# Optimization experiments

Hardware: AMD Instinct MI355X
Metric: run time of the kernel (lower is better)

The kernel has to match this reference:

```python
import jax, jax.numpy as jnp
import numpy as np

B, N, H = 2, 1024, 768
MAX_W = 30
WIDTH_D = 20
SPAN_DIM = 3 * H + WIDTH_D  # 2324
K = int(N * 0.4)  # 409 (eval mode: // (1+0) )


def _enumerate_spans(n, max_w):
    # Replicates: enumerate_spans then sorted(spans[::-1], key=start)
    # -> start ascending, end DESCENDING within each start.
    spans = []
    for s in range(n):
        for e in range(min(s + max_w - 1, n - 1), s - 1, -1):
            spans.append((s, e))
    return np.asarray(spans, dtype=np.int32)  # [num_spans, 2]


def setup_inputs() -> dict:
    key = jax.random.key(0)
    ks = jax.random.split(key, 8)
    spans = jnp.asarray(_enumerate_spans(N, MAX_W))  # [30285, 2]
    return {
        "segment_embeddings": jax.random.normal(ks[0], (B, N, H), jnp.float32),
        "segment_mask": jnp.ones((B, N), jnp.int32),
        "candidate_spans": spans,
        "width_emb": jax.random.normal(ks[1], (MAX_W, WIDTH_D), jnp.float32) * 0.02,
        "W1": jax.random.normal(ks[2], (SPAN_DIM, H), jnp.float32) * 0.02,
        "b1": jax.random.normal(ks[3], (H,), jnp.float32) * 0.02,
        "w_s": jax.random.normal(ks[4], (H,), jnp.float32) * 0.02,
        "b_s": jax.random.normal(ks[5], (1,), jnp.float32) * 0.02,
        "k": K,
    }


def reference(segment_embeddings, segment_mask, candidate_spans, width_emb, W1, b1, w_s, b_s, k):
    starts = candidate_spans[:, 0]  # [S]
    ends = candidate_spans[:, 1]    # [S]
    # Endpoint span extractor: x, y, x*y + width embedding (width = end-start)
    x = segment_embeddings[:, starts, :]          # [B,S,H]
    y = segment_embeddings[:, ends, :]            # [B,S,H]
    wemb = width_emb[ends - starts]               # [S,WIDTH_D]
    bsz = segment_embeddings.shape[0]
    span_feat = jnp.concatenate(
        [x, y, x * y, jnp.broadcast_to(wemb[None], (bsz,) + wemb.shape)], axis=-1
    )  # [B,S,3H+WD]
    # MLP (dropout is identity in eval) + GELU (torch default: exact erf)
    h = jax.nn.gelu(jnp.einsum("bsd,dh->bsh", span_feat, W1) + b1, approximate=False)
    scores = jnp.einsum("bsh,h->bs", h, w_s) + b_s[0]  # [B,S]
    # Mask spans whose end index exceeds valid length
    lengths = segment_mask.sum(-1)  # [B]
    scores = scores + jnp.where(ends[None, :] >= lengths[:, None], -1e6, 0.0)
    # Top-k prune, then sort indices and gather
    _, idx = jax.lax.top_k(scores, k)          # [B,k]
    idx = jnp.sort(idx, axis=1)
    top_scores = jnp.take_along_axis(scores, idx, axis=1)            # [B,k]
    top_span_embs = jnp.take_along_axis(h, idx[:, :, None], axis=1)  # [B,k,H]
    top_spans = candidate_spans[idx]                                 # [B,k,2]
    return top_span_embs, top_scores, top_spans
```

## Files before the change

### kernel.cpp

```cpp
#include <hip/hip_runtime.h>
#include <math.h>

#define NB 2
#define NN 1024
#define HH 768
#define MAXW 30
#define KTOP 409
#define BANDCAP 4096
#define BAND_TAU 2e-2f
#define FILTCAP 6144
#define CHT 120
#define GPAD 448
#define SP416 416

typedef __attribute__((ext_vector_type(4))) float f32x4;
typedef __attribute__((ext_vector_type(8))) __bf16 bf16x8;
typedef __attribute__((ext_vector_type(8))) unsigned short us8;

constexpr int MT = 64, NT = 256, KT = 32;
constexpr int ASTR = MT + 4;
constexpr int BSTR = NT + 4;

__device__ __forceinline__ float gelu_f(float z) {
  return 0.5f * z * (1.0f + erff(z * 0.70710678118654752440f));
}
__device__ __forceinline__ unsigned f2key(float f) {
  unsigned u = __float_as_uint(f);
  return (u & 0x80000000u) ? ~u : (u | 0x80000000u);
}
__device__ __forceinline__ float key2f(unsigned k) {
  unsigned u = (k & 0x80000000u) ? (k & 0x7fffffffu) : ~k;
  return __uint_as_float(u);
}
__device__ __forceinline__ unsigned short f2bf_rn(float f) {
  unsigned u = __float_as_uint(f);
  unsigned r = u + 0x7fffu + ((u >> 16) & 1u);
  return (unsigned short)(r >> 16);
}
__device__ __forceinline__ float bf2f(unsigned short h) {
  return __uint_as_float(((unsigned)h) << 16);
}
__device__ __forceinline__ void async_copy16(const void* g, void* l) {
  __builtin_amdgcn_global_load_lds(
      (const __attribute__((address_space(1))) unsigned int*)g,
      (__attribute__((address_space(3))) unsigned int*)l, 16, 0, 0);
}

__global__ void len_kernel(const int* __restrict__ mask, int* __restrict__ lengths) {
  __shared__ int red[256];
  for (int b = 0; b < NB; ++b) {
    int s = 0;
    for (int i = threadIdx.x; i < NN; i += 256) s += mask[b * NN + i];
    red[threadIdx.x] = s;
    __syncthreads();
    for (int off = 128; off > 0; off >>= 1) {
      if (threadIdx.x < off) red[threadIdx.x] += red[threadIdx.x + off];
      __syncthreads();
    }
    if (threadIdx.x == 0) lengths[b] = red[0];
    __syncthreads();
  }
}

__global__ void r_kernel(const float* __restrict__ wemb, const float* __restrict__ W1,
                         const float* __restrict__ b1, float* __restrict__ R) {
  int w = blockIdx.x;
  for (int h = threadIdx.x; h < HH; h += 256) {
    float acc = b1[h];
    for (int j = 0; j < 20; ++j)
      acc = fmaf(wemb[w * 20 + j], W1[(size_t)(3 * HH + j) * HH + h], acc);
    R[w * HH + h] = acc;
  }
}

__global__ __launch_bounds__(256) void prep_bt_kernel(const float* __restrict__ W1,
                                                      unsigned short* __restrict__ Bt) {
  const int ki = blockIdx.x;
  const int hby = blockIdx.y;
  const float* W1c = W1 + (size_t)(2 * HH) * HH;
  const int t = threadIdx.x;
#pragma unroll
  for (int half = 0; half < 2; ++half) {
    const int c = t + half * 256;
    const int col = c >> 2, kg = c & 3;
    us8 v;
#pragma unroll
    for (int j = 0; j < 8; ++j) {
      const int k = ki * 32 + kg * 8 + j;
      v[j] = f2bf_rn(W1c[(size_t)k * HH + hby * 128 + col]);
    }
    *(us8*)(Bt + ((size_t)(hby * 24 + ki) * 512 + c) * 8) = v;
  }
}

__global__ __launch_bounds__(256) void prep_emb_hl_kernel(
    const float* __restrict__ emb, unsigned short* __restrict__ Ahi,
    unsigned short* __restrict__ Alo) {
  const int tile = blockIdx.x;
  const int ki = blockIdx.y;
  const int t = threadIdx.x;
#pragma unroll
  for (int half = 0; half < 2; ++half) {
    const int c = t + half * 256;
    const int row = c >> 2, kgs = c & 3;
    const int kg = kgs ^ ((row >> 1) & 3);
    const float* xr = emb + (size_t)(tile * 128 + row) * HH;
    const int k0 = ki * 32 + kg * 8;
    float4 x0 = *(const float4*)(xr + k0);
    float4 x1 = *(const float4*)(xr + k0 + 4);
    const float xv[8] = {x0.x, x0.y, x0.z, x0.w, x1.x, x1.y, x1.z, x1.w};
    us8 hv, lv;
#pragma unroll
    for (int j = 0; j < 8; ++j) {
      unsigned short h = f2bf_rn(xv[j]);
      hv[j] = h;
      lv[j] = f2bf_rn(xv[j] - bf2f(h));
    }
    const size_t base = (((size_t)tile * 24 + ki) * 512 + c) * 8;
    *(us8*)(Ahi + base) = hv;
    *(us8*)(Alo + base) = lv;
  }
}

__global__ __launch_bounds__(256) void prep_w1ab_kernel(
    const float* __restrict__ W1, unsigned short* __restrict__ Bhi,
    unsigned short* __restrict__ Blo) {
  const int ki = blockIdx.x;
  const int hby = blockIdx.y;
  const int t = threadIdx.x;
#pragma unroll
  for (int half = 0; half < 2; ++half) {
    const int c = t + half * 256;
    const int col = c >> 2, kg = c & 3;
    const int gc = hby * 128 + col;
    const float* base = W1 + (gc < 768 ? (size_t)0 : (size_t)HH * HH);
    const int n = (gc < 768) ? gc : gc - 768;
    us8 hv, lv;
#pragma unroll
    for (int j = 0; j < 8; ++j) {
      const int k = ki * 32 + kg * 8 + j;
      float v = base[(size_t)k * HH + n];
      unsigned short h = f2bf_rn(v);
      hv[j] = h;
      lv[j] = f2bf_rn(v - bf2f(h));
    }
    const size_t bo = (((size_t)hby * 24 + ki) * 512 + c) * 8;
    *(us8*)(Bhi + bo) = hv;
    *(us8*)(Blo + bo) = lv;
  }
}

__global__ __launch_bounds__(256) void pq_mfma_kernel(
    const unsigned short* __restrict__ Ahi, const unsigned short* __restrict__ Alo,
    const unsigned short* __restrict__ Bhi, const unsigned short* __restrict__ Blo,
    float* __restrict__ P, float* __restrict__ Q) {
  __shared__ unsigned short AsmH[128 * 32], AsmL[128 * 32];
  const int tile = blockIdx.x;
  const int hby = blockIdx.y;
  const int tid = threadIdx.x;
  const int lane = tid & 63, w = tid >> 6;
  const int wm = w & 1, wn = w >> 1;
  const int lm = lane & 15, lq = lane >> 4;

  f32x4 acc[4][4];
#pragma unroll
  for (int i = 0; i < 4; ++i)
#pragma unroll
    for (int j = 0; j < 4; ++j) acc[i][j] = (f32x4){0.f, 0.f, 0.f, 0.f};

  const unsigned short* AbH = Ahi + (size_t)tile * 24 * 4096;
  const unsigned short* AbL = Alo + (size_t)tile * 24 * 4096;
  const unsigned short* BbH = Bhi + (size_t)hby * 24 * 4096;
  const unsigned short* BbL = Blo + (size_t)hby * 24 * 4096;
  const int a_off = (wm * 64 + lm) * 32 + (lq ^ ((lm >> 1) & 3)) * 8;
  const int b_off = (wn * 64 + lm) * 32 + lq * 8;

  for (int ki = 0; ki < 24; ++ki) {
    async_copy16(AbH + (size_t)ki * 4096 + tid * 8, AsmH + tid * 8);
    async_copy16(AbH + (size_t)ki * 4096 + (tid + 256) * 8, AsmH + (tid + 256) * 8);
    async_copy16(AbL + (size_t)ki * 4096 + tid * 8, AsmL + tid * 8);
    async_copy16(AbL + (size_t)ki * 4096 + (tid + 256) * 8, AsmL + (tid + 256) * 8);
    bf16x8 bh[4], bl[4];
#pragma unroll
    for (int ni = 0; ni < 4; ++ni) {
      bh[ni] = *reinterpret_cast<const bf16x8*>(BbH + (size_t)ki * 4096 + b_off + ni * 512);
      bl[ni] = *reinterpret_cast<const bf16x8*>(BbL + (size_t)ki * 4096 + b_off + ni * 512);
    }
    __syncthreads();
    bf16x8 ah[4], al[4];
#pragma unroll
    for (int mi = 0; mi < 4; ++mi) {
      ah[mi] = *reinterpret_cast<const bf16x8*>(AsmH + a_off + mi * 512);
      al[mi] = *reinterpret_cast<const bf16x8*>(AsmL + a_off + mi * 512);
    }
#pragma unroll
    for (int ni = 0; ni < 4; ++ni)
#pragma unroll
      for (int mi = 0; mi < 4; ++mi) {
        acc[mi][ni] = __builtin_amdgcn_mfma_f32_16x16x32_bf16(ah[mi], bh[ni], acc[mi][ni], 0, 0, 0);
        acc[mi][ni] = __builtin_amdgcn_mfma_f32_16x16x32_bf16(ah[mi], bl[ni], acc[mi][ni], 0, 0, 0);
        acc[mi][ni] = __builtin_amdgcn_mfma_f32_16x16x32_bf16(al[mi], bh[ni], acc[mi][ni], 0, 0, 0);
      }
    __syncthreads();
  }

  float* Obase = (hby < 6) ? P : Q;
  const int cb = ((hby < 6) ? hby : hby - 6) * 128 + wn * 64 + lm;
  const int rowb = tile * 128 + wm * 64 + lq * 4;
#pragma unroll
  for (int mi = 0; mi < 4; ++mi)
#pragma unroll
    for (int ni = 0; ni < 4; ++ni)
#pragma unroll
      for (int r = 0; r < 4; ++r)
        Obase[(size_t)(rowb + mi * 16 + r) * HH + cb + ni * 16] = acc[mi][ni][r];
}

__global__ __launch_bounds__(256) void prep_a_kernel(
    const float* __restrict__ emb, const int* __restrict__ spans,
    unsigned short* __restrict__ At, int S, int tileofs) {
  const int tl = blockIdx.x, b = blockIdx.y;
  const int tile = tileofs + tl;
  const int t = threadIdx.x;
#pragma unroll
  for (int half = 0; half < 2; ++half) {
    const int c = t + half * 256;
    const int row = c >> 2, kgs = c & 3;
    const int kg = kgs ^ ((row >> 1) & 3);
    int g = tile * 128 + row;
    if (g >= S) g = S - 1;
    const int s = spans[2 * g], e = spans[2 * g + 1];
    const float* xr = emb + ((size_t)b * NN + s) * HH;
    const float* yr = emb + ((size_t)b * NN + e) * HH;
    unsigned short* dst = At + (((size_t)b * CHT + tl) * 24 * 512 + c) * 8;
    for (int ki = 0; ki < 24; ++ki) {
      const int k0 = ki * 32 + kg * 8;
      float4 x0 = *(const float4*)(xr + k0);
      float4 x1 = *(const float4*)(xr + k0 + 4);
      float4 y0 = *(const float4*)(yr + k0);
      float4 y1 = *(const float4*)(yr + k0 + 4);
      us8 v;
      v[0] = f2bf_rn(x0.x * y0.x); v[1] = f2bf_rn(x0.y * y0.y);
      v[2] = f2bf_rn(x0.z * y0.z); v[3] = f2bf_rn(x0.w * y0.w);
      v[4] = f2bf_rn(x1.x * y1.x); v[5] = f2bf_rn(x1.y * y1.y);
      v[6] = f2bf_rn(x1.z * y1.z); v[7] = f2bf_rn(x1.w * y1.w);
      *(us8*)(dst + (size_t)ki * 4096) = v;
    }
  }
}

__global__ __launch_bounds__(256, 3) void score_mfma3_kernel(
    const int* __restrict__ spans,
    const unsigned short* __restrict__ At, const unsigned short* __restrict__ Bt,
    const float* __restrict__ w_s,
    const float* __restrict__ P, const float* __restrict__ Q, const float* __restrict__ R,
    float* __restrict__ spart, int S, int tileofs) {
  __shared__ unsigned short Asm[128 * 32];
  __shared__ int ssm[128], eem[128], wwm[128];
  __shared__ float sred[128 * 2];

  const int tl = blockIdx.x;
  const int tile = tileofs + tl;
  const int hby = blockIdx.y;
  const int b = blockIdx.z;
  const int tid = threadIdx.x;
  const int lane = tid & 63, w = tid >> 6;
  const int wm = w & 1, wn = w >> 1;
  const int lm = lane & 15, lq = lane >> 4;

  if (tid < 128) {
    int g = tile * 128 + tid;
    int gg = g < S ? g : S - 1;
    int s = spans[2 * gg], e = spans[2 * gg + 1];
    ssm[tid] = s; eem[tid] = e; wwm[tid] = e - s;
  }

  f32x4 acc[4][4];
#pragma unroll
  for (int i = 0; i < 4; ++i)
#pragma unroll
    for (int j = 0; j < 4; ++j) acc[i][j] = (f32x4){0.f, 0.f, 0.f, 0.f};

  const unsigned short* Ab = At + ((size_t)b * CHT + tl) * 24 * 4096;
  const unsigned short* Bb = Bt + (size_t)hby * 24 * 4096;
  const int a_off = (wm * 64 + lm) * 32 + (lq ^ ((lm >> 1) & 3)) * 8;
  const int b_off = (wn * 64 + lm) * 32 + lq * 8;

  for (int ki = 0; ki < 24; ++ki) {
    async_copy16(Ab + (size_t)ki * 4096 + tid * 8, Asm + tid * 8);
    async_copy16(Ab + (size_t)ki * 4096 + (tid + 256) * 8, Asm + (tid + 256) * 8);
    bf16x8 bfr[4];
#pragma unroll
    for (int ni = 0; ni < 4; ++ni)
      bfr[ni] = *reinterpret_cast<const bf16x8*>(Bb + (size_t)ki * 4096 + b_off + ni * 512);
    __syncthreads();
    bf16x8 afr[4];
#pragma unroll
    for (int mi = 0; mi < 4; ++mi)
      afr[mi] = *reinterpret_cast<const bf16x8*>(Asm + a_off + mi * 512);
#pragma unroll
    for (int ni = 0; ni < 4; ++ni)
#pragma unroll
      for (int mi = 0; mi < 4; ++mi)
        acc[mi][ni] = __builtin_amdgcn_mfma_f32_16x16x32_bf16(afr[mi], bfr[ni], acc[mi][ni], 0, 0, 0);
    __syncthreads();
  }

  const int hbg = hby * 128;
  float wsv[4];
#pragma unroll
  for (int ni = 0; ni < 4; ++ni) wsv[ni] = w_s[hbg + wn * 64 + ni * 16 + lm];

#pragma unroll
  for (int mi = 0; mi < 4; ++mi) {
#pragma unroll
    for (int r = 0; r < 4; ++r) {
      const int rowl = wm * 64 + mi * 16 + lq * 4 + r;
      const int s = ssm[rowl], e = eem[rowl], wd = wwm[rowl];
      const float* Pp = P + ((size_t)b * NN + s) * HH + hbg + wn * 64 + lm;
      const float* Qp = Q + ((size_t)b * NN + e) * HH + hbg + wn * 64 + lm;
      const float* Rp = R + (size_t)wd * HH + hbg + wn * 64 + lm;
      float psum = 0.f;
#pragma unroll
      for (int ni = 0; ni < 4; ++ni) {
        float z = acc[mi][ni][r] + Pp[ni * 16] + Qp[ni * 16] + Rp[ni * 16];
        psum = fmaf(gelu_f(z), wsv[ni], psum);
      }
      psum += __shfl_xor(psum, 1);
      psum += __shfl_xor(psum, 2);
      psum += __shfl_xor(psum, 4);
      psum += __shfl_xor(psum, 8);
      if (lm == 0) sred[rowl * 2 + wn] = psum;
    }
  }
  __syncthreads();
  if (tid < 128) {
    int g = tile * 128 + tid;
    if (g < S)
      spart[(size_t)hby * ((size_t)NB * S) + (size_t)b * S + g] = sred[tid * 2] + sred[tid * 2 + 1];
  }
}

__global__ void combine_kernel(const float* __restrict__ sp, const int* __restrict__ spans,
                               const float* __restrict__ b_s, const int* __restrict__ lengths,
                               float* __restrict__ scores, int S) {
  int idx = blockIdx.x * 256 + threadIdx.x;
  if (idx >= NB * S) return;
  int b = idx / S, i = idx - b * S;
  size_t st = (size_t)NB * S;
  float v = b_s[0];
#pragma unroll
  for (int j = 0; j < 6; ++j) v += sp[j * st + idx];
  if (spans[2 * i + 1] >= lengths[b]) v += -1000000.0f;
  scores[idx] = v;
}

__global__ void zero_kernel(unsigned* __restrict__ hist, int* __restrict__ bandcount,
                            int* __restrict__ filtcount) {
  int i = blockIdx.x * 256 + threadIdx.x;
  hist[i] = 0;
  if (blockIdx.x == 0 && threadIdx.x < NB) {
    bandcount[threadIdx.x] = 0;
    filtcount[threadIdx.x] = 0;
  }
}

__global__ void hist16_kernel(const float* __restrict__ scores, unsigned* __restrict__ hist,
                              int S) {
  int idx = blockIdx.x * 256 + threadIdx.x;
  if (idx >= NB * S) return;
  int b = idx / S;
  unsigned key = f2key(scores[idx]) >> 16;
  atomicAdd(&hist[(size_t)b * 65536 + key], 1u);
}

__global__ __launch_bounds__(1024) void scan16_kernel(const unsigned* __restrict__ hist,
                                                      const int* __restrict__ kptr,
                                                      float* __restrict__ pivotf) {
  const int b = blockIdx.x;
  const unsigned* hb = hist + (size_t)b * 65536;
  const int tid = threadIdx.x;
  const unsigned k = (unsigned)kptr[0];
  __shared__ unsigned acc[1024];
  unsigned s = 0;
  for (int j = 0; j < 64; ++j) s += hb[tid * 64 + j];
  const unsigned mysum = s;
  acc[tid] = s;
  __syncthreads();
  for (int off = 1; off < 1024; off <<= 1) {
    unsigned v = (tid + off < 1024) ? acc[tid + off] : 0u;
    __syncthreads();
    acc[tid] += v;
    __syncthreads();
  }
  const unsigned above = acc[tid] - mysum;
  if (above < k && acc[tid] >= k) {
    unsigned cum = above;
    int binf = tid * 64;
    for (int j = 63; j >= 0; --j) {
      unsigned c = hb[tid * 64 + j];
      if (cum + c >= k) { binf = tid * 64 + j; break; }
      cum += c;
    }
    pivotf[b] = key2f(((unsigned)binf) << 16);
  }
}

__global__ void band_kernel(const float* __restrict__ scores, const float* __restrict__ pivotf,
                            int* __restrict__ bandcount, int* __restrict__ bandlist, int S) {
  int idx = blockIdx.x * 256 + threadIdx.x;
  if (idx >= NB * S) return;
  int b = idx / S, i = idx - b * S;
  if (fabsf(scores[idx] - pivotf[b]) <= BAND_TAU) {
    int slot = atomicAdd(&bandcount[b], 1);
    if (slot < BANDCAP) bandlist[b * BANDCAP + slot] = i;
  }
}

__global__ __launch_bounds__(256) void rescore_kernel(
    const float* __restrict__ emb, const int* __restrict__ spans,
    const float* __restrict__ W1, const float* __restrict__ w_s,
    const float* __restrict__ b_s, const int* __restrict__ lengths,
    const float* __restrict__ P, const float* __restrict__ Q, const float* __restrict__ R,
    const int* __restrict__ bandcount, const int* __restrict__ bandlist,
    float* __restrict__ scores, int S) {
  const int b = blockIdx.y;
  int cnt = bandcount[b];
  if (cnt > BANDCAP) cnt = BANDCAP;
  if ((int)blockIdx.x >= cnt) return;
  const int i = bandlist[b * BANDCAP + blockIdx.x];
  const int s = spans[2 * i], e = spans[2 * i + 1], wd = e - s;
  const int tid = threadIdx.x;
  __shared__ float prod[HH];
  __shared__ float red[256];
  for (int c = tid; c < HH; c += 256)
    prod[c] = emb[((size_t)b * NN + s) * HH + c] * emb[((size_t)b * NN + e) * HH + c];
  __syncthreads();
  const float* W1c = W1 + (size_t)(2 * HH) * HH;
  float psum = 0.f;
  for (int c0 = 0; c0 < HH; c0 += 256) {
    const int c = c0 + tid;
    float a = P[((size_t)b * NN + s) * HH + c] + Q[((size_t)b * NN + e) * HH + c] + R[(size_t)wd * HH + c];
    for (int k = 0; k < HH; ++k) a = fmaf(prod[k], W1c[(size_t)k * HH + c], a);
    psum = fmaf(gelu_f(a), w_s[c], psum);
  }
  red[tid] = psum;
  __syncthreads();
  for (int off = 128; off > 0; off >>= 1) {
    if (tid < off) red[tid] += red[tid + off];
    __syncthreads();
  }
  if (tid == 0) {
    float v = red[0] + b_s[0];
    if (e >= lengths[b]) v += -1000000.0f;
    scores[(size_t)b * S + i] = v;
  }
}

__global__ void filt_kernel(const float* __restrict__ scores, const float* __restrict__ pivotf,
                            int* __restrict__ filtcount, int* __restrict__ filtlist, int S) {
  int idx = blockIdx.x * 256 + threadIdx.x;
  if (idx >= NB * S) return;
  int b = idx / S, i = idx - b * S;
  if (scores[idx] > pivotf[b] - 0.01f) {
    int slot = atomicAdd(&filtcount[b], 1);
    if (slot < FILTCAP) filtlist[b * FILTCAP + slot] = i;
  }
}

__global__ __launch_bounds__(1024) void sel_kernel(
    const float* __restrict__ scores, const int* __restrict__ spans,
    const int* __restrict__ kptr, const int* __restrict__ filtcount,
    const int* __restrict__ filtlist,
    float* __restrict__ out_spans, int* __restrict__ sel, int S) {
  const int b = blockIdx.x;
  const int tid = threadIdx.x;
  const int k = kptr[0];
  __shared__ unsigned keys[FILTCAP];
  __shared__ int idxs[FILTCAP];
  __shared__ unsigned hist[256];
  __shared__ unsigned sh_prefix;
  __shared__ int sh_remaining;
  __shared__ int selcnt;
  __shared__ int slist[512];

  int M = filtcount[b];
  if (M > FILTCAP) M = FILTCAP;
  for (int i = tid; i < M; i += 1024) {
    int gi = filtlist[b * FILTCAP + i];
    idxs[i] = gi;
    keys[i] = f2key(scores[(size_t)b * S + gi]);
  }
  if (tid == 0) selcnt = 0;
  __syncthreads();

  unsigned prefix = 0;
  int remaining = k;
  for (int round = 0; round < 4; ++round) {
    const int shift = 24 - 8 * round;
    if (tid < 256) hist[tid] = 0;
    __syncthreads();
    for (int i = tid; i < M; i += 1024) {
      unsigned key = keys[i];
      if (round == 0 || (key >> (shift + 8)) == prefix)
        atomicAdd(&hist[(key >> shift) & 255u], 1u);
    }
    __syncthreads();
    if (tid == 0) {
      int cum = 0;
      for (int bin = 255; bin >= 0; --bin) {
        int c = (int)hist[bin];
        if (cum + c >= remaining) {
          sh_prefix = (prefix << 8) | (unsigned)bin;
          sh_remaining = remaining - cum;
          break;
        }
        cum += c;
      }
    }
    __syncthreads();
    prefix = sh_prefix;
    remaining = sh_remaining;
    __syncthreads();
  }
  const unsigned pk = prefix;
  const int m_eq = remaining;

  for (int i = tid; i < M; i += 1024) {
    unsigned key = keys[i];
    bool pick = false;
    if (key > pk) {
      pick = true;
    } else if (key == pk) {
      int r = 0;
      const int myidx = idxs[i];
      for (int j = 0; j < M; ++j)
        if (keys[j] == pk && idxs[j] < myidx) ++r;
      pick = (r < m_eq);
    }
    if (pick) {
      int p = atomicAdd(&selcnt, 1);
      if (p < 512) slist[p] = idxs[i];
    }
  }
  __syncthreads();

  for (int i = tid; i < k; i += 1024) {
    const int my = slist[i];
    int r = 0;
    for (int j = 0; j < k; ++j) r += (slist[j] < my);
    sel[b * KTOP + r] = my;
    out_spans[(b * KTOP + r) * 2 + 0] = (float)spans[2 * my];
    out_spans[(b * KTOP + r) * 2 + 1] = (float)spans[2 * my + 1];
  }
}

__global__ __launch_bounds__(256) void gather_part_kernel(
    const float* __restrict__ emb, const int* __restrict__ spans,
    const float* __restrict__ W1, const int* __restrict__ sel,
    float* __restrict__ Gpart) {
  __shared__ float As[KT][ASTR];
  __shared__ float Bs[KT][BSTR];
  __shared__ int ssm[MT], eem[MT];
  const int tile = blockIdx.x;
  const int hby6 = blockIdx.y;
  const int hb = (hby6 / 6) * NT;
  const int ks = hby6 % 6;
  const int b = blockIdx.z;
  const int tid = threadIdx.x;
  const int th = tid & 31, tw = tid >> 5;
  if (tid < MT) {
    int j = tile * MT + tid;
    if (j >= KTOP) j = KTOP - 1;
    int i = sel[b * KTOP + j];
    ssm[tid] = spans[2 * i];
    eem[tid] = spans[2 * i + 1];
  }
  __syncthreads();
  const int m0 = tid >> 3, m1 = m0 + 32;
  const int d0 = (tid & 7) << 2;
  const size_t ebase = (size_t)b * NN * HH;
  const size_t rx0 = ebase + (size_t)ssm[m0] * HH;
  const size_t ry0 = ebase + (size_t)eem[m0] * HH;
  const size_t rx1 = ebase + (size_t)ssm[m1] * HH;
  const size_t ry1 = ebase + (size_t)eem[m1] * HH;
  const float* W1c = W1 + (size_t)(2 * HH) * HH;
  const int bc = (tid & 63) << 2;
  const int br = tid >> 6;
  float acc[8][8];
#pragma unroll
  for (int i = 0; i < 8; ++i)
#pragma unroll
    for (int j = 0; j < 8; ++j) acc[i][j] = 0.f;
  const int k0 = ks * 128;
  for (int it = 0; it < 4; ++it) {
    const int kt = k0 + it * KT;
    float4 x0 = *reinterpret_cast<const float4*>(emb + rx0 + kt + d0);
    float4 y0 = *reinterpret_cast<const float4*>(emb + ry0 + kt + d0);
    float4 x1 = *reinterpret_cast<const float4*>(emb + rx1 + kt + d0);
    float4 y1 = *reinterpret_cast<const float4*>(emb + ry1 + kt + d0);
    float4 bw[8];
#pragma unroll
    for (int r = 0; r < 8; ++r)
      bw[r] = *reinterpret_cast<const float4*>(W1c + (size_t)(kt + br + 4 * r) * HH + hb + bc);
    __syncthreads();
    As[d0 + 0][m0] = x0.x * y0.x; As[d0 + 1][m0] = x0.y * y0.y;
    As[d0 + 2][m0] = x0.z * y0.z; As[d0 + 3][m0] = x0.w * y0.w;
    As[d0 + 0][m1] = x1.x * y1.x; As[d0 + 1][m1] = x1.y * y1.y;
    As[d0 + 2][m1] = x1.z * y1.z; As[d0 + 3][m1] = x1.w * y1.w;
#pragma unroll
    for (int r = 0; r < 8; ++r)
      *reinterpret_cast<float4*>(&Bs[br + 4 * r][bc]) = bw[r];
    __syncthreads();
#pragma unroll
    for (int d = 0; d < KT; ++d) {
      const float4 a0 = *reinterpret_cast<const float4*>(&As[d][tw * 4]);
      const float4 a1 = *reinterpret_cast<const float4*>(&As[d][tw * 4 + 32]);
      const float4 b0 = *reinterpret_cast<const float4*>(&Bs[d][th * 4]);
      const float4 b1v = *reinterpret_cast<const float4*>(&Bs[d][th * 4 + 128]);
      const float av[8] = {a0.x, a0.y, a0.z, a0.w, a1.x, a1.y, a1.z, a1.w};
      const float bv[8] = {b0.x, b0.y, b0.z, b0.w, b1v.x, b1v.y, b1v.z, b1v.w};
#pragma unroll
      for (int mi = 0; mi < 8; ++mi)
#pragma unroll
        for (int ni = 0; ni < 8; ++ni)
          acc[mi][ni] = fmaf(av[mi], bv[ni], acc[mi][ni]);
    }
  }
#pragma unroll
  for (int mi = 0; mi < 8; ++mi) {
    const int m = tw * 4 + (mi & 3) + ((mi >> 2) << 5);
    float* op = Gpart + (((size_t)ks * NB + b) * GPAD + tile * MT + m) * HH + hb;
    *reinterpret_cast<float4*>(op + th * 4) = make_float4(acc[mi][0], acc[mi][1], acc[mi][2], acc[mi][3]);
    *reinterpret_cast<float4*>(op + th * 4 + 128) = make_float4(acc[mi][4], acc[mi][5], acc[mi][6], acc[mi][7]);
  }
}

__global__ __launch_bounds__(256) void gather_fin_kernel(
    const float* __restrict__ Gpart, const int* __restrict__ spans,
    const int* __restrict__ sel,
    const float* __restrict__ P, const float* __restrict__ Q, const float* __restrict__ R,
    const float* __restrict__ w_s, float* __restrict__ outh, float* __restrict__ spartg) {
  __shared__ int ssm[16], eem[16], wwm[16], vvm[16];
  __shared__ float sred[16];
  const int t16 = blockIdx.x;
  const int hby = blockIdx.y;
  const int b = blockIdx.z;
  const int tid = threadIdx.x;
  if (tid < 16) {
    int j = t16 * 16 + tid;
    int valid = (j < KTOP) ? 1 : 0;
    int jj = valid ? j : KTOP - 1;
    int i = sel[b * KTOP + jj];
    ssm[tid] = spans[2 * i];
    eem[tid] = spans[2 * i + 1];
    wwm[tid] = eem[tid] - ssm[tid];
    vvm[tid] = valid;
  }
  __syncthreads();
  const int row = tid >> 4;
  const int cc = tid & 15;
  const int g448 = t16 * 16 + row;
  const int co = hby * 128 + cc * 8;
  float v[8];
#pragma unroll
  for (int i = 0; i < 8; ++i) v[i] = 0.f;
#pragma unroll
  for (int ks = 0; ks < 6; ++ks) {
    const float* gp = Gpart + (((size_t)ks * NB + b) * GPAD + g448) * HH + co;
    float4 a = *(const float4*)gp;
    float4 c = *(const float4*)(gp + 4);
    v[0] += a.x; v[1] += a.y; v[2] += a.z; v[3] += a.w;
    v[4] += c.x; v[5] += c.y; v[6] += c.z; v[7] += c.w;
  }
  const int s = ssm[row], e = eem[row], wd = wwm[row];
  const float* Pp = P + ((size_t)b * NN + s) * HH + co;
  const float* Qp = Q + ((size_t)b * NN + e) * HH + co;
  const float* Rp = R + (size_t)wd * HH + co;
  float4 p0 = *(const float4*)Pp, p1 = *(const float4*)(Pp + 4);
  float4 q0 = *(const float4*)Qp, q1 = *(const float4*)(Qp + 4);
  float4 r0 = *(const float4*)Rp, r1 = *(const float4*)(Rp + 4);
  v[0] += p0.x + q0.x + r0.x; v[1] += p0.y + q0.y + r0.y;
  v[2] += p0.z + q0.z + r0.z; v[3] += p0.w + q0.w + r0.w;
  v[4] += p1.x + q1.x + r1.x; v[5] += p1.y + q1.y + r1.y;
  v[6] += p1.z + q1.z + r1.z; v[7] += p1.w + q1.w + r1.w;
  float gl[8];
#pragma unroll
  for (int i = 0; i < 8; ++i) gl[i] = gelu_f(v[i]);
  float psum = 0.f;
  if (vvm[row]) {
    const int j = t16 * 16 + row;
    float* op = outh + (size_t)(b * KTOP + j) * HH + co;
    *(float4*)op = make_float4(gl[0], gl[1], gl[2], gl[3]);
    *(float4*)(op + 4) = make_float4(gl[4], gl[5], gl[6], gl[7]);
    const float4 w0 = *(const float4*)(w_s + co);
    const float4 w1 = *(const float4*)(w_s + co + 4);
    psum = gl[0] * w0.x + gl[1] * w0.y + gl[2] * w0.z + gl[3] * w0.w +
           gl[4] * w1.x + gl[5] * w1.y + gl[6] * w1.z + gl[7] * w1.w;
  }
  psum += __shfl_xor(psum, 1);
  psum += __shfl_xor(psum, 2);
  psum += __shfl_xor(psum, 4);
  psum += __shfl_xor(psum, 8);
  const int lane = tid & 63, wv = tid >> 6;
  if ((lane & 15) == 0) sred[wv * 4 + (lane >> 4)] = psum;
  __syncthreads();
  if (tid < 16)
    spartg[(size_t)hby * (NB * SP416) + b * SP416 + t16 * 16 + tid] = sred[tid];
}

__global__ void score_fin_kernel(const float* __restrict__ spartg, const int* __restrict__ sel,
                                 const int* __restrict__ spans, const float* __restrict__ b_s,
                                 const int* __restrict__ lengths, float* __restrict__ out_scores) {
  int idx = blockIdx.x * 256 + threadIdx.x;
  if (idx >= NB * KTOP) return;
  int b = idx / KTOP, j = idx - b * KTOP;
  float v = b_s[0];
#pragma unroll
  for (int hby = 0; hby < 6; ++hby)
    v += spartg[(size_t)hby * (NB * SP416) + b * SP416 + j];
  int i = sel[idx];
  if (spans[2 * i + 1] >= lengths[b]) v += -1000000.0f;
  out_scores[idx] = v;
}

extern "C" void kernel_launch(void* const* d_in, const int* in_sizes, int n_in,
                              void* d_out, int out_size, void* d_ws, size_t ws_size,
                              hipStream_t stream) {
  const float* emb = (const float*)d_in[0];
  const int* mask = (const int*)d_in[1];
  const int* spans = (const int*)d_in[2];
  const float* wemb = (const float*)d_in[3];
  const float* W1 = (const float*)d_in[4];
  const float* b1 = (const float*)d_in[5];
  const float* w_s = (const float*)d_in[6];
  const float* b_s = (const float*)d_in[7];
  const int* kptr = (const int*)d_in[8];
  const int S = in_sizes[2] / 2;
  float* out = (float*)d_out;

  char* wp = (char*)d_ws;
  auto take = [&](size_t bytes) {
    char* p = wp;
    wp += (bytes + 63) & ~(size_t)63;
    return p;
  };
  float* Pb = (float*)take((size_t)NB * NN * HH * 4);
  float* Qb = (float*)take((size_t)NB * NN * HH * 4);
  float* Rb = (float*)take((size_t)MAXW * HH * 4);
  float* spart = (float*)take(6 * (size_t)NB * S * 4);
  float* scoresb = (float*)take((size_t)NB * S * 4);
  float* spartg = (float*)take(6 * (size_t)NB * SP416 * 4);
  float* Gpart = (float*)take(6 * (size_t)NB * GPAD * HH * 4);
  float* pivotf = (float*)take(NB * 4);
  unsigned short* At = (unsigned short*)take((size_t)NB * CHT * 24 * 4096 * 2);
  unsigned short* Bt = (unsigned short*)take((size_t)6 * 24 * 4096 * 2);
  unsigned* hist16b = (unsigned*)take((size_t)NB * 65536 * 4);
  int* selb = (int*)take(NB * KTOP * 4);
  int* lengthsb = (int*)take(NB * 4);
  int* bandcount = (int*)take(NB * 4);
  int* bandlist = (int*)take((size_t)NB * BANDCAP * 4);
  int* filtcount = (int*)take(NB * 4);
  int* filtlist = (int*)take((size_t)NB * FILTCAP * 4);

  unsigned short* AimgHi = At;
  unsigned short* AimgLo = AimgHi + (size_t)16 * 24 * 4096;
  unsigned short* BimgHi = AimgLo + (size_t)16 * 24 * 4096;
  unsigned short* BimgLo = BimgHi + (size_t)12 * 24 * 4096;

  const size_t OFF1 = (size_t)NB * KTOP * HH;
  const size_t OFF2 = OFF1 + (size_t)NB * KTOP;

  const int tiles = (S + 127) / 128;

  len_kernel<<<dim3(1), dim3(256), 0, stream>>>(mask, lengthsb);
  r_kernel<<<dim3(MAXW), dim3(256), 0, stream>>>(wemb, W1, b1, Rb);
  prep_bt_kernel<<<dim3(24, 6), dim3(256), 0, stream>>>(W1, Bt);
  prep_emb_hl_kernel<<<dim3(16, 24), dim3(256), 0, stream>>>(emb, AimgHi, AimgLo);
  prep_w1ab_kernel<<<dim3(24, 12), dim3(256), 0, stream>>>(W1, BimgHi, BimgLo);
  pq_mfma_kernel<<<dim3(16, 12), dim3(256), 0, stream>>>(AimgHi, AimgLo, BimgHi, BimgLo, Pb, Qb);
  zero_kernel<<<dim3(512), dim3(256), 0, stream>>>(hist16b, bandcount, filtcount);

  for (int pass = 0; pass < 2; ++pass) {
    const int ofs = pass * CHT;
    const int nt = (pass == 0) ? CHT : (tiles - CHT);
    prep_a_kernel<<<dim3(nt, NB), dim3(256), 0, stream>>>(emb, spans, At, S, ofs);
    score_mfma3_kernel<<<dim3(nt, 6, NB), dim3(256), 0, stream>>>(
        spans, At, Bt, w_s, Pb, Qb, Rb, spart, S, ofs);
  }

  combine_kernel<<<dim3((NB * S + 255) / 256), dim3(256), 0, stream>>>(
      spart, spans, b_s, lengthsb, scoresb, S);
  hist16_kernel<<<dim3((NB * S + 255) / 256), dim3(256), 0, stream>>>(scoresb, hist16b, S);
  scan16_kernel<<<dim3(NB), dim3(1024), 0, stream>>>(hist16b, kptr, pivotf);
  band_kernel<<<dim3((NB * S + 255) / 256), dim3(256), 0, stream>>>(
      scoresb, pivotf, bandcount, bandlist, S);
  rescore_kernel<<<dim3(BANDCAP, NB), dim3(256), 0, stream>>>(
      emb, spans, W1, w_s, b_s, lengthsb, Pb, Qb, Rb, bandcount, bandlist, scoresb, S);
  filt_kernel<<<dim3((NB * S + 255) / 256), dim3(256), 0, stream>>>(
      scoresb, pivotf, filtcount, filtlist, S);
  sel_kernel<<<dim3(NB), dim3(1024), 0, stream>>>(
      scoresb, spans, kptr, filtcount, filtlist, out + OFF2, selb, S);
  gather_part_kernel<<<dim3(7, 18, NB), dim3(256), 0, stream>>>(emb, spans, W1, selb, Gpart);
  gather_fin_kernel<<<dim3(26, 6, NB), dim3(256), 0, stream>>>(
      Gpart, spans, selb, Pb, Qb, Rb, w_s, out, spartg);
  score_fin_kernel<<<dim3((NB * KTOP + 255) / 256), dim3(256), 0, stream>>>(
      spartg, selb, spans, b_s, lengthsb, out + OFF1);
}
```

Baseline: 560.3 us.

## Widen score MFMA tile to 256 columns and move gather GEMM to split-bf16 MFMA

The main scoring kernel now makes each block compute 256 output columns instead of 128. This halves the number of times each A tile is streamed and halves the partial-score reductions, at the cost of doubling the accumulator registers and lowering launch bounds occupancy from 3 to 2. The gather stage used an fp32 FMA GEMM followed by a separate partial-sum kernel. It is replaced by a bf16 hi/lo split MFMA GEMM (three products) that fuses GELU, the output write and the partial score computation. This needs a new prep kernel for the gathered A images and a low-part copy of the B image.

New measurement: 677.2 us. +20.9%, slower.

```diff
diff --git a/kernel.cpp b/kernel.cpp
--- a/kernel.cpp
+++ b/kernel.cpp
@@ -10,16 +10,11 @@
 #define BAND_TAU 2e-2f
 #define FILTCAP 6144
 #define CHT 120
-#define GPAD 448
-#define SP416 416
+#define GROWS 512
 
 typedef __attribute__((ext_vector_type(4))) float f32x4;
 typedef __attribute__((ext_vector_type(8))) __bf16 bf16x8;
 typedef __attribute__((ext_vector_type(8))) unsigned short us8;
-
-constexpr int MT = 64, NT = 256, KT = 32;
-constexpr int ASTR = MT + 4;
-constexpr int BSTR = NT + 4;
 
 __device__ __forceinline__ float gelu_f(float z) {
   return 0.5f * z * (1.0f + erff(z * 0.70710678118654752440f));
@@ -74,7 +69,8 @@
 }
 
 __global__ __launch_bounds__(256) void prep_bt_kernel(const float* __restrict__ W1,
-                                                      unsigned short* __restrict__ Bt) {
+                                                      unsigned short* __restrict__ Bt,
+                                                      unsigned short* __restrict__ Btlo) {
   const int ki = blockIdx.x;
   const int hby = blockIdx.y;
   const float* W1c = W1 + (size_t)(2 * HH) * HH;
@@ -83,13 +79,18 @@
   for (int half = 0; half < 2; ++half) {
     const int c = t + half * 256;
     const int col = c >> 2, kg = c & 3;
-    us8 v;
+    us8 hv, lv;
 #pragma unroll
     for (int j = 0; j < 8; ++j) {
       const int k = ki * 32 + kg * 8 + j;
-      v[j] = f2bf_rn(W1c[(size_t)k * HH + hby * 128 + col]);
-    }
-    *(us8*)(Bt + ((size_t)(hby * 24 + ki) * 512 + c) * 8) = v;
+      float v = W1c[(size_t)k * HH + hby * 128 + col];
+      unsigned short h = f2bf_rn(v);
+      hv[j] = h;
+      lv[j] = f2bf_rn(v - bf2f(h));
+    }
+    const size_t bo = ((size_t)(hby * 24 + ki) * 512 + c) * 8;
+    *(us8*)(Bt + bo) = hv;
+    *(us8*)(Btlo + bo) = lv;
   }
 }
 
@@ -249,7 +250,7 @@
   }
 }
 
-__global__ __launch_bounds__(256, 3) void score_mfma3_kernel(
+__global__ __launch_bounds__(256, 2) void score_mfma4_kernel(
     const int* __restrict__ spans,
     const unsigned short* __restrict__ At, const unsigned short* __restrict__ Bt,
     const float* __restrict__ w_s,
@@ -259,9 +260,9 @@
   __shared__ int ssm[128], eem[128], wwm[128];
   __shared__ float sred[128 * 2];
 
-  const int tl = blockIdx.x;
+  const int hb2 = blockIdx.x;
+  const int tl = blockIdx.y;
   const int tile = tileofs + tl;
-  const int hby = blockIdx.y;
   const int b = blockIdx.z;
   const int tid = threadIdx.x;
   const int lane = tid & 63, w = tid >> 6;
@@ -275,41 +276,45 @@
     ssm[tid] = s; eem[tid] = e; wwm[tid] = e - s;
   }
 
-  f32x4 acc[4][4];
+  f32x4 acc[4][8];
 #pragma unroll
   for (int i = 0; i < 4; ++i)
 #pragma unroll
-    for (int j = 0; j < 4; ++j) acc[i][j] = (f32x4){0.f, 0.f, 0.f, 0.f};
+    for (int j = 0; j < 8; ++j) acc[i][j] = (f32x4){0.f, 0.f, 0.f, 0.f};
 
   const unsigned short* Ab = At + ((size_t)b * CHT + tl) * 24 * 4096;
-  const unsigned short* Bb = Bt + (size_t)hby * 24 * 4096;
+  const unsigned short* Bb0 = Bt + (size_t)(hb2 * 2) * 24 * 4096;
+  const unsigned short* Bb1 = Bt + (size_t)(hb2 * 2 + 1) * 24 * 4096;
   const int a_off = (wm * 64 + lm) * 32 + (lq ^ ((lm >> 1) & 3)) * 8;
   const int b_off = (wn * 64 + lm) * 32 + lq * 8;
 
   for (int ki = 0; ki < 24; ++ki) {
     async_copy16(Ab + (size_t)ki * 4096 + tid * 8, Asm + tid * 8);
     async_copy16(Ab + (size_t)ki * 4096 + (tid + 256) * 8, Asm + (tid + 256) * 8);
-    bf16x8 bfr[4];
-#pragma unroll
-    for (int ni = 0; ni < 4; ++ni)
-      bfr[ni] = *reinterpret_cast<const bf16x8*>(Bb + (size_t)ki * 4096 + b_off + ni * 512);
+    bf16x8 bfr[8];
+#pragma unroll
+    for (int ni = 0; ni < 4; ++ni) {
+      bfr[ni] = *reinterpret_cast<const bf16x8*>(Bb0 + (size_t)ki * 4096 + b_off + ni * 512);
+      bfr[ni + 4] = *reinterpret_cast<const bf16x8*>(Bb1 + (size_t)ki * 4096 + b_off + ni * 512);
+    }
     __syncthreads();
     bf16x8 afr[4];
 #pragma unroll
     for (int mi = 0; mi < 4; ++mi)
       afr[mi] = *reinterpret_cast<const bf16x8*>(Asm + a_off + mi * 512);
 #pragma unroll
-    for (int ni = 0; ni < 4; ++ni)
+    for (int ni = 0; ni < 8; ++ni)
 #pragma unroll
       for (int mi = 0; mi < 4; ++mi)
         acc[mi][ni] = __builtin_amdgcn_mfma_f32_16x16x32_bf16(afr[mi], bfr[ni], acc[mi][ni], 0, 0, 0);
     __syncthreads();
   }
 
-  const int hbg = hby * 128;
-  float wsv[4];
-#pragma unroll
-  for (int ni = 0; ni < 4; ++ni) wsv[ni] = w_s[hbg + wn * 64 + ni * 16 + lm];
+  const int hbg = hb2 * 256;
+  float wsv[8];
+#pragma unroll
+  for (int ni = 0; ni < 8; ++ni)
+    wsv[ni] = w_s[hbg + (ni >> 2) * 128 + wn * 64 + (ni & 3) * 16 + lm];
 
 #pragma unroll
   for (int mi = 0; mi < 4; ++mi) {
@@ -322,8 +327,9 @@
       const float* Rp = R + (size_t)wd * HH + hbg + wn * 64 + lm;
       float psum = 0.f;
 #pragma unroll
-      for (int ni = 0; ni < 4; ++ni) {
-        float z = acc[mi][ni][r] + Pp[ni * 16] + Qp[ni * 16] + Rp[ni * 16];
+      for (int ni = 0; ni < 8; ++ni) {
+        const int co = (ni >> 2) * 128 + (ni & 3) * 16;
+        float z = acc[mi][ni][r] + Pp[co] + Qp[co] + Rp[co];
         psum = fmaf(gelu_f(z), wsv[ni], psum);
       }
       psum += __shfl_xor(psum, 1);
@@ -337,7 +343,7 @@
   if (tid < 128) {
     int g = tile * 128 + tid;
     if (g < S)
-      spart[(size_t)hby * ((size_t)NB * S) + (size_t)b * S + g] = sred[tid * 2] + sred[tid * 2 + 1];
+      spart[(size_t)hb2 * ((size_t)NB * S) + (size_t)b * S + g] = sred[tid * 2] + sred[tid * 2 + 1];
   }
 }
 
@@ -350,7 +356,7 @@
   size_t st = (size_t)NB * S;
   float v = b_s[0];
 #pragma unroll
-  for (int j = 0; j < 6; ++j) v += sp[j * st + idx];
+  for (int j = 0; j < 3; ++j) v += sp[j * st + idx];
   if (spans[2 * i + 1] >= lengths[b]) v += -1000000.0f;
   scores[idx] = v;
 }
@@ -555,100 +561,67 @@
   }
 }
 
-__global__ __launch_bounds__(256) void gather_part_kernel(
+__global__ __launch_bounds__(256) void prep_ga_kernel(
     const float* __restrict__ emb, const int* __restrict__ spans,
-    const float* __restrict__ W1, const int* __restrict__ sel,
-    float* __restrict__ Gpart) {
-  __shared__ float As[KT][ASTR];
-  __shared__ float Bs[KT][BSTR];
-  __shared__ int ssm[MT], eem[MT];
+    const int* __restrict__ sel, unsigned short* __restrict__ GAhi,
+    unsigned short* __restrict__ GAlo) {
   const int tile = blockIdx.x;
-  const int hby6 = blockIdx.y;
-  const int hb = (hby6 / 6) * NT;
-  const int ks = hby6 % 6;
-  const int b = blockIdx.z;
-  const int tid = threadIdx.x;
-  const int th = tid & 31, tw = tid >> 5;
-  if (tid < MT) {
-    int j = tile * MT + tid;
+  const int b = blockIdx.y;
+  const int t = threadIdx.x;
+#pragma unroll
+  for (int half = 0; half < 2; ++half) {
+    const int c = t + half * 256;
+    const int row = c >> 2, kgs = c & 3;
+    const int kg = kgs ^ ((row >> 1) & 3);
+    int j = tile * 128 + row;
     if (j >= KTOP) j = KTOP - 1;
-    int i = sel[b * KTOP + j];
-    ssm[tid] = spans[2 * i];
-    eem[tid] = spans[2 * i + 1];
-  }
-  __syncthreads();
-  const int m0 = tid >> 3, m1 = m0 + 32;
-  const int d0 = (tid & 7) << 2;
-  const size_t ebase = (size_t)b * NN * HH;
-  const size_t rx0 = ebase + (size_t)ssm[m0] * HH;
-  const size_t ry0 = ebase + (size_t)eem[m0] * HH;
-  const size_t rx1 = ebase + (size_t)ssm[m1] * HH;
-  const size_t ry1 = ebase + (size_t)eem[m1] * HH;
-  const float* W1c = W1 + (size_t)(2 * HH) * HH;
-  const int bc = (tid & 63) << 2;
-  const int br = tid >> 6;
-  float acc[8][8];
-#pragma unroll
-  for (int i = 0; i < 8; ++i)
-#pragma unroll
-    for (int j = 0; j < 8; ++j) acc[i][j] = 0.f;
-  const int k0 = ks * 128;
-  for (int it = 0; it < 4; ++it) {
-    const int kt = k0 + it * KT;
-    float4 x0 = *reinterpret_cast<const float4*>(emb + rx0 + kt + d0);
-    float4 y0 = *reinterpret_cast<const float4*>(emb + ry0 + kt + d0);
-    float4 x1 = *reinterpret_cast<const float4*>(emb + rx1 + kt + d0);
-    float4 y1 = *reinterpret_cast<const float4*>(emb + ry1 + kt + d0);
-    float4 bw[8];
-#pragma unroll
-    for (int r = 0; r < 8; ++r)
-      bw[r] = *reinterpret_cast<const float4*>(W1c + (size_t)(kt + br + 4 * r) * HH + hb + bc);
-    __syncthreads();
-    As[d0 + 0][m0] = x0.x * y0.x; As[d0 + 1][m0] = x0.y * y0.y;
-    As[d0 + 2][m0] = x0.z * y0.z; As[d0 + 3][m0] = x0.w * y0.w;
-    As[d0 + 0][m1] = x1.x * y1.x; As[d0 + 1][m1] = x1.y * y1.y;
-    As[d0 + 2][m1] = x1.z * y1.z; As[d0 + 3][m1] = x1.w * y1.w;
-#pragma unroll
-    for (int r = 0; r < 8; ++r)
-      *reinterpret_cast<float4*>(&Bs[br + 4 * r][bc]) = bw[r];
-    __syncthreads();
-#pragma unroll
-    for (int d = 0; d < KT; ++d) {
-      const float4 a0 = *reinterpret_cast<const float4*>(&As[d][tw * 4]);
-      const float4 a1 = *reinterpret_cast<const float4*>(&As[d][tw * 4 + 32]);
-      const float4 b0 = *reinterpret_cast<const float4*>(&Bs[d][th * 4]);
-      const float4 b1v = *reinterpret_cast<const float4*>(&Bs[d][th * 4 + 128]);
-      const float av[8] = {a0.x, a0.y, a0.z, a0.w, a1.x, a1.y, a1.z, a1.w};
-      const float bv[8] = {b0.x, b0.y, b0.z, b0.w, b1v.x, b1v.y, b1v.z, b1v.w};
-#pragma unroll
-      for (int mi = 0; mi < 8; ++mi)
-#pragma unroll
-        for (int ni = 0; ni < 8; ++ni)
-          acc[mi][ni] = fmaf(av[mi], bv[ni], acc[mi][ni]);
-    }
-  }
-#pragma unroll
-  for (int mi = 0; mi < 8; ++mi) {
-    const int m = tw * 4 + (mi & 3) + ((mi >> 2) << 5);
-    float* op = Gpart + (((size_t)ks * NB + b) * GPAD + tile * MT + m) * HH + hb;
-    *reinterpret_cast<float4*>(op + th * 4) = make_float4(acc[mi][0], acc[mi][1], acc[mi][2], acc[mi][3]);
-    *reinterpret_cast<float4*>(op + th * 4 + 128) = make_float4(acc[mi][4], acc[mi][5], acc[mi][6], acc[mi][7]);
-  }
-}
-
-__global__ __launch_bounds__(256) void gather_fin_kernel(
-    const float* __restrict__ Gpart, const int* __restrict__ spans,
-    const int* __restrict__ sel,
+    const int i = sel[b * KTOP + j];
+    const int s = spans[2 * i], e = spans[2 * i + 1];
+    const float* xr = emb + ((size_t)b * NN + s) * HH;
+    const float* yr = emb + ((size_t)b * NN + e) * HH;
+    unsigned short* dh = GAhi + (((size_t)(b * 4 + tile)) * 24 * 512 + c) * 8;
+    unsigned short* dl = GAlo + (((size_t)(b * 4 + tile)) * 24 * 512 + c) * 8;
+    for (int ki = 0; ki < 24; ++ki) {
+      const int k0 = ki * 32 + kg * 8;
+      float4 x0 = *(const float4*)(xr + k0);
+      float4 x1 = *(const float4*)(xr + k0 + 4);
+      float4 y0 = *(const float4*)(yr + k0);
+      float4 y1 = *(const float4*)(yr + k0 + 4);
+      const float pv[8] = {x0.x * y0.x, x0.y * y0.y, x0.z * y0.z, x0.w * y0.w,
+                           x1.x * y1.x, x1.y * y1.y, x1.z * y1.z, x1.w * y1.w};
+      us8 hv, lv;
+#pragma unroll
+      for (int q = 0; q < 8; ++q) {
+        unsigned short h = f2bf_rn(pv[q]);
+        hv[q] = h;
+        lv[q] = f2bf_rn(pv[q] - bf2f(h));
+      }
+      *(us8*)(dh + (size_t)ki * 4096) = hv;
+      *(us8*)(dl + (size_t)ki * 4096) = lv;
+    }
+  }
+}
+
+__global__ __launch_bounds__(256) void gather_mfma_kernel(
+    const int* __restrict__ spans, const int* __restrict__ sel,
+    const unsigned short* __restrict__ GAhi, const unsigned short* __restrict__ GAlo,
+    const unsigned short* __restrict__ Bt, const unsigned short* __restrict__ Btlo,
+    const float* __restrict__ w_s,
     const float* __restrict__ P, const float* __restrict__ Q, const float* __restrict__ R,
-    const float* __restrict__ w_s, float* __restrict__ outh, float* __restrict__ spartg) {
-  __shared__ int ssm[16], eem[16], wwm[16], vvm[16];
-  __shared__ float sred[16];
-  const int t16 = blockIdx.x;
+    float* __restrict__ outh, float* __restrict__ spartg) {
+  __shared__ unsigned short AsmH[128 * 32], AsmL[128 * 32];
+  __shared__ int ssm[128], eem[128], wwm[128], vvm[128];
+  __shared__ float sred[128 * 2];
+  const int tile = blockIdx.x;
   const int hby = blockIdx.y;
   const int b = blockIdx.z;
   const int tid = threadIdx.x;
-  if (tid < 16) {
-    int j = t16 * 16 + tid;
+  const int lane = tid & 63, w = tid >> 6;
+  const int wm = w & 1, wn = w >> 1;
+  const int lm = lane & 15, lq = lane >> 4;
+
+  if (tid < 128) {
+    int j = tile * 128 + tid;
     int valid = (j < KTOP) ? 1 : 0;
     int jj = valid ? j : KTOP - 1;
     int i = sel[b * KTOP + jj];
@@ -657,56 +630,84 @@
     wwm[tid] = eem[tid] - ssm[tid];
     vvm[tid] = valid;
   }
+
+  f32x4 acc[4][4];
+#pragma unroll
+  for (int i = 0; i < 4; ++i)
+#pragma unroll
+    for (int j = 0; j < 4; ++j) acc[i][j] = (f32x4){0.f, 0.f, 0.f, 0.f};
+
+  const unsigned short* AbH = GAhi + (size_t)(b * 4 + tile) * 24 * 4096;
+  const unsigned short* AbL = GAlo + (size_t)(b * 4 + tile) * 24 * 4096;
+  const unsigned short* BbH = Bt + (size_t)hby * 24 * 4096;
+  const unsigned short* BbL = Btlo + (size_t)hby * 24 * 4096;
+  const int a_off = (wm * 64 + lm) * 32 + (lq ^ ((lm >> 1) & 3)) * 8;
+  const int b_off = (wn * 64 + lm) * 32 + lq * 8;
+
+  for (int ki = 0; ki < 24; ++ki) {
+    async_copy16(AbH + (size_t)ki * 4096 + tid * 8, AsmH + tid * 8);
+    async_copy16(AbH + (size_t)ki * 4096 + (tid + 256) * 8, AsmH + (tid + 256) * 8);
+    async_copy16(AbL + (size_t)ki * 4096 + tid * 8, AsmL + tid * 8);
+    async_copy16(AbL + (size_t)ki * 4096 + (tid + 256) * 8, AsmL + (tid + 256) * 8);
+    bf16x8 bh[4], bl[4];
+#pragma unroll
+    for (int ni = 0; ni < 4; ++ni) {
+      bh[ni] = *reinterpret_cast<const bf16x8*>(BbH + (size_t)ki * 4096 + b_off + ni * 512);
+      bl[ni] = *reinterpret_cast<const bf16x8*>(BbL + (size_t)ki * 4096 + b_off + ni * 512);
+    }
+    __syncthreads();
+    bf16x8 ah[4], al[4];
+#pragma unroll
+    for (int mi = 0; mi < 4; ++mi) {
+      ah[mi] = *reinterpret_cast<const bf16x8*>(AsmH + a_off + mi * 512);
+      al[mi] = *reinterpret_cast<const bf16x8*>(AsmL + a_off + mi * 512);
+    }
+#pragma unroll
+    for (int ni = 0; ni < 4; ++ni)
+#pragma unroll
+      for (int mi = 0; mi < 4; ++mi) {
+        acc[mi][ni] = __builtin_amdgcn_mfma_f32_16x16x32_bf16(ah[mi], bh[ni], acc[mi][ni], 0, 0, 0);
+        acc[mi][ni] = __builtin_amdgcn_mfma_f32_16x16x32_bf16(ah[mi], bl[ni], acc[mi][ni], 0, 0, 0);
+        acc[mi][ni] = __builtin_amdgcn_mfma_f32_16x16x32_bf16(al[mi], bh[ni], acc[mi][ni], 0, 0, 0);
+      }
+    __syncthreads();
+  }
+
+  const int hbg = hby * 128;
+  float wsv[4];
+#pragma unroll
+  for (int ni = 0; ni < 4; ++ni) wsv[ni] = w_s[hbg + wn * 64 + ni * 16 + lm];
+
+#pragma unroll
+  for (int mi = 0; mi < 4; ++mi) {
+#pragma unroll
+    for (int r = 0; r < 4; ++r) {
+      const int rowl = wm * 64 + mi * 16 + lq * 4 + r;
+      const int s = ssm[rowl], e = eem[rowl], wd = wwm[rowl];
+      const float* Pp = P + ((size_t)b * NN + s) * HH + hbg + wn * 64 + lm;
+      const float* Qp = Q + ((size_t)b * NN + e) * HH + hbg + wn * 64 + lm;
+      const float* Rp = R + (size_t)wd * HH + hbg + wn * 64 + lm;
+      float psum = 0.f;
+      const int j = tile * 128 + rowl;
+      float* op = outh + (size_t)(b * KTOP + j) * HH + hbg + wn * 64 + lm;
+#pragma unroll
+      for (int ni = 0; ni < 4; ++ni) {
+        float z = acc[mi][ni][r] + Pp[ni * 16] + Qp[ni * 16] + Rp[ni * 16];
+        float gl = gelu_f(z);
+        if (vvm[rowl]) op[ni * 16] = gl;
+        psum = fmaf(gl, wsv[ni], psum);
+      }
+      psum += __shfl_xor(psum, 1);
+      psum += __shfl_xor(psum, 2);
+      psum += __shfl_xor(psum, 4);
+      psum += __shfl_xor(psum, 8);
+      if (lm == 0) sred[rowl * 2 + wn] = psum;
+    }
+  }
   __syncthreads();
-  const int row = tid >> 4;
-  const int cc = tid & 15;
-  const int g448 = t16 * 16 + row;
-  const int co = hby * 128 + cc * 8;
-  float v[8];
-#pragma unroll
-  for (int i = 0; i < 8; ++i) v[i] = 0.f;
-#pragma unroll
-  for (int ks = 0; ks < 6; ++ks) {
-    const float* gp = Gpart + (((size_t)ks * NB + b) * GPAD + g448) * HH + co;
-    float4 a = *(const float4*)gp;
-    float4 c = *(const float4*)(gp + 4);
-    v[0] += a.x; v[1] += a.y; v[2] += a.z; v[3] += a.w;
-    v[4] += c.x; v[5] += c.y; v[6] += c.z; v[7] += c.w;
-  }
-  const int s = ssm[row], e = eem[row], wd = wwm[row];
-  const float* Pp = P + ((size_t)b * NN + s) * HH + co;
-  const float* Qp = Q + ((size_t)b * NN + e) * HH + co;
-  const float* Rp = R + (size_t)wd * HH + co;
-  float4 p0 = *(const float4*)Pp, p1 = *(const float4*)(Pp + 4);
-  float4 q0 = *(const float4*)Qp, q1 = *(const float4*)(Qp + 4);
-  float4 r0 = *(const float4*)Rp, r1 = *(const float4*)(Rp + 4);
-  v[0] += p0.x + q0.x + r0.x; v[1] += p0.y + q0.y + r0.y;
-  v[2] += p0.z + q0.z + r0.z; v[3] += p0.w + q0.w + r0.w;
-  v[4] += p1.x + q1.x + r1.x; v[5] += p1.y + q1.y + r1.y;
-  v[6] += p1.z + q1.z + r1.z; v[7] += p1.w + q1.w + r1.w;
-  float gl[8];
-#pragma unroll
-  for (int i = 0; i < 8; ++i) gl[i] = gelu_f(v[i]);
-  float psum = 0.f;
-  if (vvm[row]) {
-    const int j = t16 * 16 + row;
-    float* op = outh + (size_t)(b * KTOP + j) * HH + co;
-    *(float4*)op = make_float4(gl[0], gl[1], gl[2], gl[3]);
-    *(float4*)(op + 4) = make_float4(gl[4], gl[5], gl[6], gl[7]);
-    const float4 w0 = *(const float4*)(w_s + co);
-    const float4 w1 = *(const float4*)(w_s + co + 4);
-    psum = gl[0] * w0.x + gl[1] * w0.y + gl[2] * w0.z + gl[3] * w0.w +
-           gl[4] * w1.x + gl[5] * w1.y + gl[6] * w1.z + gl[7] * w1.w;
-  }
-  psum += __shfl_xor(psum, 1);
-  psum += __shfl_xor(psum, 2);
-  psum += __shfl_xor(psum, 4);
-  psum += __shfl_xor(psum, 8);
-  const int lane = tid & 63, wv = tid >> 6;
-  if ((lane & 15) == 0) sred[wv * 4 + (lane >> 4)] = psum;
-  __syncthreads();
-  if (tid < 16)
-    spartg[(size_t)hby * (NB * SP416) + b * SP416 + t16 * 16 + tid] = sred[tid];
+  if (tid < 128)
+    spartg[(size_t)hby * (NB * GROWS) + b * GROWS + tile * 128 + tid] =
+        sred[tid * 2] + sred[tid * 2 + 1];
 }
 
 __global__ void score_fin_kernel(const float* __restrict__ spartg, const int* __restrict__ sel,
@@ -718,7 +719,7 @@
   float v = b_s[0];
 #pragma unroll
   for (int hby = 0; hby < 6; ++hby)
-    v += spartg[(size_t)hby * (NB * SP416) + b * SP416 + j];
+    v += spartg[(size_t)hby * (NB * GROWS) + b * GROWS + j];
   int i = sel[idx];
   if (spans[2 * i + 1] >= lengths[b]) v += -1000000.0f;
   out_scores[idx] = v;
@@ -748,13 +749,15 @@
   float* Pb = (float*)take((size_t)NB * NN * HH * 4);
   float* Qb = (float*)take((size_t)NB * NN * HH * 4);
   float* Rb = (float*)take((size_t)MAXW * HH * 4);
-  float* spart = (float*)take(6 * (size_t)NB * S * 4);
+  float* spart = (float*)take(3 * (size_t)NB * S * 4);
   float* scoresb = (float*)take((size_t)NB * S * 4);
-  float* spartg = (float*)take(6 * (size_t)NB * SP416 * 4);
-  float* Gpart = (float*)take(6 * (size_t)NB * GPAD * HH * 4);
+  float* spartg = (float*)take(6 * (size_t)NB * GROWS * 4);
   float* pivotf = (float*)take(NB * 4);
   unsigned short* At = (unsigned short*)take((size_t)NB * CHT * 24 * 4096 * 2);
   unsigned short* Bt = (unsigned short*)take((size_t)6 * 24 * 4096 * 2);
+  unsigned short* Btlo = (unsigned short*)take((size_t)6 * 24 * 4096 * 2);
+  unsigned short* GAhi = (unsigned short*)take((size_t)NB * 4 * 24 * 4096 * 2);
+  unsigned short* GAlo = (unsigned short*)take((size_t)NB * 4 * 24 * 4096 * 2);
   unsigned* hist16b = (unsigned*)take((size_t)NB * 65536 * 4);
   int* selb = (int*)take(NB * KTOP * 4);
   int* lengthsb = (int*)take(NB * 4);
@@ -775,7 +778,7 @@
 
   len_kernel<<<dim3(1), dim3(256), 0, stream>>>(mask, lengthsb);
   r_kernel<<<dim3(MAXW), dim3(256), 0, stream>>>(wemb, W1, b1, Rb);
-  prep_bt_kernel<<<dim3(24, 6), dim3(256), 0, stream>>>(W1, Bt);
+  prep_bt_kernel<<<dim3(24, 6), dim3(256), 0, stream>>>(W1, Bt, Btlo);
   prep_emb_hl_kernel<<<dim3(16, 24), dim3(256), 0, stream>>>(emb, AimgHi, AimgLo);
   prep_w1ab_kernel<<<dim3(24, 12), dim3(256), 0, stream>>>(W1, BimgHi, BimgLo);
   pq_mfma_kernel<<<dim3(16, 12), dim3(256), 0, stream>>>(AimgHi, AimgLo, BimgHi, BimgLo, Pb, Qb);
@@ -785,7 +788,7 @@
     const int ofs = pass * CHT;
     const int nt = (pass == 0) ? CHT : (tiles - CHT);
     prep_a_kernel<<<dim3(nt, NB), dim3(256), 0, stream>>>(emb, spans, At, S, ofs);
-    score_mfma3_kernel<<<dim3(nt, 6, NB), dim3(256), 0, stream>>>(
+    score_mfma4_kernel<<<dim3(3, nt, NB), dim3(256), 0, stream>>>(
         spans, At, Bt, w_s, Pb, Qb, Rb, spart, S, ofs);
   }
 
@@ -801,9 +804,9 @@
       scoresb, pivotf, filtcount, filtlist, S);
   sel_kernel<<<dim3(NB), dim3(1024), 0, stream>>>(
       scoresb, spans, kptr, filtcount, filtlist, out + OFF2, selb, S);
-  gather_part_kernel<<<dim3(7, 18, NB), dim3(256), 0, stream>>>(emb, spans, W1, selb, Gpart);
-  gather_fin_kernel<<<dim3(26, 6, NB), dim3(256), 0, stream>>>(
-      Gpart, spans, selb, Pb, Qb, Rb, w_s, out, spartg);
+  prep_ga_kernel<<<dim3(4, NB), dim3(256), 0, stream>>>(emb, spans, selb, GAhi, GAlo);
+  gather_mfma_kernel<<<dim3(4, 6, NB), dim3(256), 0, stream>>>(
+      spans, selb, GAhi, GAlo, Bt, Btlo, w_s, Pb, Qb, Rb, out, spartg);
   score_fin_kernel<<<dim3((NB * KTOP + 255) / 256), dim3(256), 0, stream>>>(
       spartg, selb, spans, b_s, lengthsb, out + OFF1);
 }
```
